# Performance work log

Measured on AMD Instinct MI355X. Metric: run time of the kernel, lower is better.

The kernel has to match this reference:

```python
import jax, jax.numpy as jnp
import numpy as np

E, H, B, S = 1024, 16, 8, 512
D = E // H
GRU_BIAS = 2.0  # config['gru_bias']
LN_EPS = 1e-5


def _pos_encoding(seq_len, dim):
    # Transformer-XL style relative positions seq_len-1 .. 0
    pos = jnp.arange(seq_len - 1, -1, -1, dtype=jnp.float32)
    inv_freq = 1.0 / (10000.0 ** (jnp.arange(0, dim, 2, dtype=jnp.float32) / dim))
    ang = pos[:, None] * inv_freq[None, :]              # [S, E/2]
    return jnp.concatenate([jnp.sin(ang), jnp.cos(ang)], axis=-1)  # [S, E]


def _layer_norm(x, g, b):
    m = x.mean(-1, keepdims=True)
    v = ((x - m) ** 2).mean(-1, keepdims=True)
    return (x - m) * jax.lax.rsqrt(v + LN_EPS) * g + b


def _rel_shift(x):
    # x: [B, H, S, S] -> Transformer-XL relative shift
    b, h, s, _ = x.shape
    x = jnp.pad(x, ((0, 0), (0, 0), (0, 0), (1, 0)))
    x = x.reshape(b, h, s + 1, s)[:, :, 1:, :]
    return x


def _gru_gate(x, y, Wr, Ur, Wz, Uz, Wg, Ug):
    # GTrXL gating: r, z gates + candidate h; z biased toward identity by GRU_BIAS
    r = jax.nn.sigmoid(y @ Wr.T + x @ Ur.T)
    z = jax.nn.sigmoid(y @ Wz.T + x @ Uz.T - GRU_BIAS)
    h = jnp.tanh(y @ Wg.T + (r * x) @ Ug.T)
    return (1.0 - z) * x + z * h


def setup_inputs() -> dict:
    rng = jax.random.key(0)
    ks = iter(jax.random.split(rng, 64))
    W = lambda *shape: jax.random.normal(next(ks), shape, jnp.float32) * 0.02
    inp = {
        "query": jax.random.normal(next(ks), (B, S, E), jnp.float32),
        "key": jax.random.normal(next(ks), (B, S, E), jnp.float32),
        "value": jax.random.normal(next(ks), (B, S, E), jnp.float32),
        "mask": jnp.tril(jnp.ones((S, S), dtype=bool)),
        "ln1_g": jnp.ones((E,), jnp.float32), "ln1_b": jnp.zeros((E,), jnp.float32),
        "ln2_g": jnp.ones((E,), jnp.float32), "ln2_b": jnp.zeros((E,), jnp.float32),
        "Wq": W(E, E), "bq": jnp.zeros((E,), jnp.float32),
        "Wk": W(E, E), "bk": jnp.zeros((E,), jnp.float32),
        "Wv": W(E, E), "bv": jnp.zeros((E,), jnp.float32),
        "Wp": W(E, E),
        "Wo": W(E, E), "bo": jnp.zeros((E,), jnp.float32),
        "u_bias": W(H, D), "v_bias": W(H, D),
        "g1_Wr": W(E, E), "g1_Ur": W(E, E), "g1_Wz": W(E, E),
        "g1_Uz": W(E, E), "g1_Wg": W(E, E), "g1_Ug": W(E, E),
        "g2_Wr": W(E, E), "g2_Ur": W(E, E), "g2_Wz": W(E, E),
        "g2_Uz": W(E, E), "g2_Wg": W(E, E), "g2_Ug": W(E, E),
        "fc_W": W(E, E), "fc_b": jnp.zeros((E,), jnp.float32),
    }
    return inp


def reference(query, key, value, mask,
              ln1_g, ln1_b, ln2_g, ln2_b,
              Wq, bq, Wk, bk, Wv, bv, Wp, Wo, bo, u_bias, v_bias,
              g1_Wr, g1_Ur, g1_Wz, g1_Uz, g1_Wg, g1_Ug,
              g2_Wr, g2_Ur, g2_Wz, g2_Uz, g2_Wg, g2_Ug,
              fc_W, fc_b):
    b, s, e = query.shape
    norm_q = _layer_norm(query, ln1_g, ln1_b)
    norm_k = _layer_norm(key, ln1_g, ln1_b)

    q = (norm_q @ Wq.T + bq).reshape(b, s, H, D)
    k = (norm_k @ Wk.T + bk).reshape(b, s, H, D)
    v = (norm_k @ Wv.T + bv).reshape(b, s, H, D)
    r = (_pos_encoding(s, e) @ Wp.T).reshape(s, H, D)      # relative pos keys

    # content term (q + u) k^T and position term (q + v) R^T with rel-shift
    AC = jnp.einsum('bshd,bthd->bhst', q + u_bias, k)
    BD = _rel_shift(jnp.einsum('bshd,thd->bhst', q + v_bias, r))
    score = (AC + BD) / jnp.sqrt(jnp.float32(D))
    score = jnp.where(mask[None, None, :, :], score, jnp.float32(-1e9))
    attn = jax.nn.softmax(score, axis=-1)
    Y = jnp.einsum('bhst,bthd->bshd', attn, v).reshape(b, s, e) @ Wo.T + bo

    out = _gru_gate(query, Y, g1_Wr, g1_Ur, g1_Wz, g1_Uz, g1_Wg, g1_Ug)
    Ef = jax.nn.relu(_layer_norm(out, ln2_g, ln2_b) @ fc_W.T + fc_b)
    out = _gru_gate(out, Ef, g2_Wr, g2_Ur, g2_Wz, g2_Uz, g2_Wg, g2_Ug)
    return out
```

## Files before the change

kernel.cpp:

```cpp
#include <hip/hip_runtime.h>

typedef unsigned short u16;
typedef __attribute__((ext_vector_type(8))) short short8;
typedef __attribute__((ext_vector_type(4))) float f32x4;

#define DEVFN __device__ __forceinline__

constexpr int Bc = 8, Sc = 512, Ec = 1024, Hc = 16, Dc = 64;

DEVFN u16 f2b(float f) {
  union { float f; unsigned u; } a; a.f = f;
  unsigned u = a.u;
  u += 0x7fffu + ((u >> 16) & 1u);
  return (u16)(u >> 16);
}
DEVFN float b2f(u16 h) {
  union { unsigned u; float f; } a; a.u = ((unsigned)h) << 16; return a.f;
}
DEVFN unsigned pack2(float a, float b) {
  return (unsigned)f2b(a) | ((unsigned)f2b(b) << 16);
}
DEVFN float wred_sum(float v) {
  #pragma unroll
  for (int o = 32; o; o >>= 1) v += __shfl_xor(v, o, 64);
  return v;
}
DEVFN void gload16(const void* g, void* l) {
  __builtin_amdgcn_global_load_lds(
      (const __attribute__((address_space(1))) void*)g,
      (__attribute__((address_space(3))) void*)l, 16, 0, 0);
}

struct PtrBundle { const float* src[18]; u16* dst[18]; };

__global__ __launch_bounds__(256) void cvtw_kernel(PtrBundle pb)
{
  int w = blockIdx.y;
  int i = blockIdx.x * 256 + threadIdx.x;
  float4 v = ((const float4*)pb.src[w])[i];
  uint2 o; o.x = pack2(v.x, v.y); o.y = pack2(v.z, v.w);
  ((uint2*)pb.dst[w])[i] = o;
}

struct GemmSeg {
  const u16* A1; const u16* A2;
  const u16* W1; const u16* W2;
  const float* bias;
  const float* bu; const float* bv;
  const u16* xB;
  const float* xF;
  const u16* zB;
  u16* o16a; u16* o16b;
  float* oF;
  int epi;
};
struct GemmDesc { GemmSeg seg[3]; };

template<int TM, int TN>
__global__ __launch_bounds__(TM == 128 ? 512 : 256) void gemm_f(GemmDesc dd)
{
  constexpr int MI = TM / 32;
  constexpr int D = (TM == 128) ? 2 : 3;
  constexpr int NBUF = D + 1;
  constexpr int BPS = 1024 / TN;
  __shared__ u16 lA[NBUF][TM * 32];
  __shared__ u16 lB[NBUF][TN * 32];
  const int tid = threadIdx.x;

  const GemmSeg s = dd.seg[blockIdx.y / BPS];
  const int n0 = (blockIdx.y % BPS) * TN;
  const int m0 = blockIdx.x * TM;
  const int wid = tid >> 6, lane = tid & 63;
  int wm, wn;
  if constexpr (TM == 128) { wm = (wid >> 2) * 64; wn = (wid & 3) * 32; }
  else                     { wm = (wid >> 1) * 32; wn = (wid & 1) * 32; }
  const int c15 = lane & 15, g = lane >> 4;
  const int arow = tid >> 2;
  const int ac8 = (((tid & 3) ^ ((tid >> 3) & 3))) * 8;
  const int gs8 = (g ^ ((c15 >> 1) & 3)) * 8;

  f32x4 acc[MI][2];
  #pragma unroll
  for (int mi = 0; mi < MI; ++mi)
    #pragma unroll
    for (int ni = 0; ni < 2; ++ni) acc[mi][ni] = {0.f, 0.f, 0.f, 0.f};

  const int nst = (s.A2 ? 2 : 1) * 32;

  auto stage = [&](int buf, int st) {
    int sg = st >> 5, k0 = (st & 31) << 5;
    const u16* Abase = (sg ? s.A2 : s.A1) + (size_t)m0 * 1024;
    const u16* Wbase = (sg ? s.W2 : s.W1) + (size_t)n0 * 1024;
    gload16(Abase + (size_t)arow * 1024 + k0 + ac8, &lA[buf][tid * 8]);
    gload16(Wbase + (size_t)arow * 1024 + k0 + ac8, &lB[buf][tid * 8]);
  };

  #pragma unroll
  for (int p = 0; p < D; ++p) stage(p, p);

  for (int st = 0; st < nst; ++st) {
    const int cur = st % NBUF;
    if constexpr (D == 2) {
      if (st + 1 < nst) asm volatile("s_waitcnt vmcnt(2)" ::: "memory");
      else              asm volatile("s_waitcnt vmcnt(0)" ::: "memory");
    } else {
      if (st + 2 < nst)      asm volatile("s_waitcnt vmcnt(4)" ::: "memory");
      else if (st + 1 < nst) asm volatile("s_waitcnt vmcnt(2)" ::: "memory");
      else                   asm volatile("s_waitcnt vmcnt(0)" ::: "memory");
    }
    __builtin_amdgcn_s_barrier();
    __builtin_amdgcn_sched_barrier(0);

    short8 afr[MI], bfr[2];
    #pragma unroll
    for (int mi = 0; mi < MI; ++mi)
      afr[mi] = *(const short8*)&lA[cur][(wm + mi * 16 + c15) * 32 + gs8];
    #pragma unroll
    for (int ni = 0; ni < 2; ++ni)
      bfr[ni] = *(const short8*)&lB[cur][(wn + ni * 16 + c15) * 32 + gs8];

    if (st + D < nst) stage((st + D) % NBUF, st + D);

    #pragma unroll
    for (int mi = 0; mi < MI; ++mi)
      #pragma unroll
      for (int ni = 0; ni < 2; ++ni)
        acc[mi][ni] = __builtin_amdgcn_mfma_f32_16x16x32_bf16(
            afr[mi], bfr[ni], acc[mi][ni], 0, 0, 0);
  }

  const int colb = n0 + wn + c15;
  const int rowb = m0 + wm + (lane >> 4) * 4;
  #pragma unroll
  for (int ni = 0; ni < 2; ++ni) {
    int col = colb + ni * 16;
    float bb = s.bias ? s.bias[col] : 0.f;
    float bu = 0.f, bvv = 0.f;
    if (s.epi == 1) { bu = s.bu[col]; bvv = s.bv[col]; }
    int hI = col >> 6, dI = col & 63;
    int kcd = (dI >> 5) & 1, gd = (dI >> 3) & 3, ed = dI & 7;
    int ntd = dI >> 4, c15d = dI & 15;
    #pragma unroll
    for (int mi = 0; mi < MI; ++mi) {
      int row0 = rowb + mi * 16;
      size_t off0 = (size_t)row0 * 1024 + col;
      float v4[4];
      #pragma unroll
      for (int q = 0; q < 4; ++q) v4[q] = acc[mi][ni][q] + bb;
      switch (s.epi) {
        case 0:
          #pragma unroll
          for (int q = 0; q < 4; ++q) s.o16a[off0 + (size_t)q * 1024] = f2b(v4[q]);
          break;
        case 1:
          #pragma unroll
          for (int q = 0; q < 4; ++q) {
            int ri = row0 + q;
            size_t off = ((size_t)hI << 18) +
                         (((size_t)(((ri >> 4) * 2 + kcd) * 16 + (ri & 15)) * 4 + gd) << 3) + ed;
            s.o16a[off] = f2b((v4[q] + bu)  * 0.125f);
            s.o16b[off] = f2b((v4[q] + bvv) * 0.125f);
          }
          break;
        case 2:
          #pragma unroll
          for (int q = 0; q < 4; ++q) s.o16a[off0 + (size_t)q * 1024] = f2b(v4[q]);
          break;
        case 3:
          #pragma unroll
          for (int q = 0; q < 4; ++q) {
            size_t off = off0 + (size_t)q * 1024;
            float sg1 = 1.f / (1.f + __expf(-v4[q]));
            s.o16a[off] = f2b(sg1 * b2f(s.xB[off]));
          }
          break;
        case 4:
          #pragma unroll
          for (int q = 0; q < 4; ++q) {
            size_t off = off0 + (size_t)q * 1024;
            float z = 1.f / (1.f + __expf(-(b2f(s.zB[off]) - 2.f)));
            float r = (1.f - z) * s.xF[off] + z * tanhf(v4[q]);
            s.oF[off] = r;
            if (s.o16a) s.o16a[off] = f2b(r);
          }
          break;
        case 5:
          #pragma unroll
          for (int q = 0; q < 4; ++q) s.o16a[off0 + (size_t)q * 1024] = f2b(fmaxf(v4[q], 0.f));
          break;
        case 6: {
          int bI = row0 >> 9, j = row0 & 511;
          int kt = j >> 6, jj = j & 63;
          int kcj = jj >> 5, gj = (jj >> 3) & 3, e0 = jj & 7;
          size_t off = ((size_t)((bI * 16 + hI) * 8 + kt) << 12) +
                       (((size_t)((ntd * 2 + kcj) * 16 + c15d) * 4 + gj) << 3) + e0;
          uint2 o; o.x = pack2(v4[0], v4[1]); o.y = pack2(v4[2], v4[3]);
          *(uint2*)(s.o16a + off) = o;
        } break;
        case 7:
          #pragma unroll
          for (int q = 0; q < 4; ++q) {
            int rj = row0 + q;
            int bI = rj >> 9, kt = (rj >> 6) & 7, jr = rj & 63;
            size_t off = ((size_t)((bI * 16 + hI) * 8 + kt) << 12) +
                         (((size_t)(((jr >> 4) * 2 + kcd) * 16 + (jr & 15)) * 4 + gd) << 3) + ed;
            s.o16a[off] = f2b(v4[q]);
          }
          break;
        case 8:
          #pragma unroll
          for (int q = 0; q < 4; ++q) {
            int t = row0 + q;
            size_t off = ((size_t)hI << 14) +
                         (((size_t)(((t >> 4) * 2 + kcd) * 16 + (t & 15)) * 4 + gd) << 3) + ed;
            s.o16a[off] = f2b(v4[q]);
          }
          break;
      }
    }
  }
}

__global__ __launch_bounds__(256) void ln_kernel(
    const float* __restrict__ x, const float* __restrict__ g,
    const float* __restrict__ bb, u16* __restrict__ out,
    u16* __restrict__ out2)
{
  const int row = blockIdx.x, t = threadIdx.x;
  float4 xv = ((const float4*)x)[(size_t)row * 256 + t];
  float s  = xv.x + xv.y + xv.z + xv.w;
  float s2 = xv.x * xv.x + xv.y * xv.y + xv.z * xv.z + xv.w * xv.w;
  s = wred_sum(s); s2 = wred_sum(s2);
  __shared__ float sh[8];
  int wid = t >> 6, lane = t & 63;
  if (lane == 0) { sh[wid] = s; sh[4 + wid] = s2; }
  __syncthreads();
  s  = sh[0] + sh[1] + sh[2] + sh[3];
  s2 = sh[4] + sh[5] + sh[6] + sh[7];
  float mean = s * (1.f / 1024.f);
  float var  = s2 * (1.f / 1024.f) - mean * mean;
  float rstd = rsqrtf(var + 1e-5f);
  float4 gv = ((const float4*)g)[t];
  float4 bv = ((const float4*)bb)[t];
  uint2 o;
  o.x = pack2((xv.x - mean) * rstd * gv.x + bv.x,
              (xv.y - mean) * rstd * gv.y + bv.y);
  o.y = pack2((xv.z - mean) * rstd * gv.z + bv.z,
              (xv.w - mean) * rstd * gv.w + bv.w);
  *(uint2*)&out[(size_t)row * 1024 + t * 4] = o;
  if (out2) {
    uint2 o2; o2.x = pack2(xv.x, xv.y); o2.y = pack2(xv.z, xv.w);
    *(uint2*)&out2[(size_t)row * 1024 + t * 4] = o2;
  }
}

__global__ __launch_bounds__(256) void posenc_kernel(u16* __restrict__ out)
{
  int idx = blockIdx.x * 256 + threadIdx.x;
  int i = idx >> 9, f = idx & 511;
  float pos = (float)(Sc - 1 - i);
  float invf = expf((float)f * -0.017988946039016f);
  float ang = pos * invf;
  out[(size_t)i * 1024 + f]       = f2b(sinf(ang));
  out[(size_t)i * 1024 + 512 + f] = f2b(cosf(ang));
}

__global__ __launch_bounds__(256) void attn_mfma(
    const u16* __restrict__ quF, const u16* __restrict__ qvF,
    const u16* __restrict__ PK, const u16* __restrict__ PVT,
    const u16* __restrict__ RF, u16* __restrict__ out)
{
  __shared__ u16 lK[2][4096];
  __shared__ u16 lVT[2][4096];
  __shared__ u16 PW[4][16 * 72];

  const int tid = threadIdx.x;
  const int wave = tid >> 6, lane = tid & 63;
  const int g = lane >> 4, c15 = lane & 15;
  const int x = blockIdx.x;
  const int h = blockIdx.y, b = blockIdx.z;
  const int qA = x, qB = 7 - x;

  const size_t pkbase = (size_t)(b * 16 + h) << 15;
  const size_t qhead  = (size_t)h << 18;
  const size_t rhead  = (size_t)h << 14;
  const size_t bh_off = ((size_t)b * Sc) * Ec + h * Dc;
  const int fchunk  = (c15 * 4 + g) * 8;
  const int fchunkS = (c15 * 4 + (g ^ ((c15 >> 1) & 3))) * 8;
  const int src8 = (tid ^ ((tid >> 3) & 3)) * 8;

  u16* pw = PW[wave];

  auto stage = [&](int buf, int kt) {
    const u16* ks = PK  + pkbase + ((size_t)kt << 12);
    const u16* vs = PVT + pkbase + ((size_t)kt << 12);
    gload16(ks + src8,        &lK[buf][tid * 8]);
    gload16(ks + 2048 + src8, &lK[buf][2048 + tid * 8]);
    gload16(vs + src8,        &lVT[buf][tid * 8]);
    gload16(vs + 2048 + src8, &lVT[buf][2048 + tid * 8]);
  };

  short8 qa[2], va[2];
  int i0w = qA * 64 + wave * 16;
  {
    int i16g = b * 32 + (i0w >> 4);
    #pragma unroll
    for (int kc = 0; kc < 2; ++kc) {
      size_t off = qhead + ((size_t)(i16g * 2 + kc) * 64) * 8 + fchunk;
      qa[kc] = *(const short8*)(quF + off);
      va[kc] = *(const short8*)(qvF + off);
    }
  }

  f32x4 oacc[4];
  #pragma unroll
  for (int t = 0; t < 4; ++t) oacc[t] = {0.f, 0.f, 0.f, 0.f};
  float m[4], l[4];
  #pragma unroll
  for (int q = 0; q < 4; ++q) { m[q] = -1e30f; l[q] = 0.f; }

  stage(0, 0);
  asm volatile("s_waitcnt vmcnt(0)" ::: "memory");
  __syncthreads();

  for (int s2 = 0; s2 < 9; ++s2) {
    const int buf = s2 & 1;
    const int kt = (s2 <= x) ? s2 : (s2 - x - 1);
    const int j0 = kt * 64;
    if (s2 < 8) {
      int ns = s2 + 1;
      stage(buf ^ 1, (ns <= x) ? ns : (ns - x - 1));
    }

    f32x4 ac[4];
    #pragma unroll
    for (int t = 0; t < 4; ++t) ac[t] = {0.f, 0.f, 0.f, 0.f};
    __builtin_amdgcn_s_setprio(1);
    #pragma unroll
    for (int kc = 0; kc < 2; ++kc)
      #pragma unroll
      for (int nt = 0; nt < 4; ++nt) {
        short8 kb = *(const short8*)&lK[buf][(nt * 2 + kc) * 512 + fchunkS];
        ac[nt] = __builtin_amdgcn_mfma_f32_16x16x32_bf16(qa[kc], kb, ac[nt], 0, 0, 0);
      }

    const int t016 = (496 - i0w + j0) >> 4;
    f32x4 e5[5];
    #pragma unroll
    for (int t = 0; t < 5; ++t) e5[t] = {0.f, 0.f, 0.f, 0.f};
    #pragma unroll
    for (int kc = 0; kc < 2; ++kc)
      #pragma unroll
      for (int nt = 0; nt < 5; ++nt) {
        int t16 = t016 + nt; t16 = t16 > 31 ? 31 : t16;
        short8 rb = *(const short8*)(RF + rhead + (size_t)(t16 * 2 + kc) * 512 + fchunk);
        e5[nt] = __builtin_amdgcn_mfma_f32_16x16x32_bf16(va[kc], rb, e5[nt], 0, 0, 0);
      }
    __builtin_amdgcn_s_setprio(0);

    float rot[5][4];
    #pragma unroll
    for (int q = 0; q < 4; ++q) {
      int src = (lane & 48) | ((15 - (g * 4 + q) + c15) & 15);
      #pragma unroll
      for (int nt = 0; nt < 5; ++nt)
        rot[nt][q] = __shfl(e5[nt][q], src, 64);
    }

    float s[4][4];
    #pragma unroll
    for (int ct = 0; ct < 4; ++ct) {
      int jcol = j0 + ct * 16 + c15;
      #pragma unroll
      for (int q = 0; q < 4; ++q) {
        int r = g * 4 + q;
        int u = 15 - r + c15;
        float bd = (u >> 4) ? rot[ct + 1][q] : rot[ct][q];
        float sv = ac[ct][q] + bd;
        s[ct][q] = (jcol <= i0w + r) ? sv : -1e30f;
      }
    }

    float mnew[4], csc[4];
    #pragma unroll
    for (int q = 0; q < 4; ++q) {
      float mx = fmaxf(fmaxf(s[0][q], s[1][q]), fmaxf(s[2][q], s[3][q]));
      #pragma unroll
      for (int o = 8; o; o >>= 1) mx = fmaxf(mx, __shfl_xor(mx, o, 64));
      mnew[q] = fmaxf(m[q], mx);
      csc[q] = __expf(m[q] - mnew[q]);
      m[q] = mnew[q];
    }
    float rs[4] = {0.f, 0.f, 0.f, 0.f};
    float p[4][4];
    #pragma unroll
    for (int ct = 0; ct < 4; ++ct)
      #pragma unroll
      for (int q = 0; q < 4; ++q) {
        p[ct][q] = __expf(s[ct][q] - mnew[q]);
        rs[q] += p[ct][q];
      }
    #pragma unroll
    for (int q = 0; q < 4; ++q) {
      float t = rs[q];
      #pragma unroll
      for (int o = 8; o; o >>= 1) t += __shfl_xor(t, o, 64);
      l[q] = l[q] * csc[q] + t;
      #pragma unroll
      for (int ct = 0; ct < 4; ++ct) oacc[ct][q] *= csc[q];
    }

    #pragma unroll
    for (int ct = 0; ct < 4; ++ct)
      #pragma unroll
      for (int q = 0; q < 4; ++q)
        pw[(g * 4 + q) * 72 + ct * 16 + c15] = f2b(p[ct][q]);

    __builtin_amdgcn_s_setprio(1);
    #pragma unroll
    for (int kc = 0; kc < 2; ++kc) {
      short8 pa = *(const short8*)&pw[c15 * 72 + kc * 32 + g * 8];
      #pragma unroll
      for (int nt = 0; nt < 4; ++nt) {
        short8 vb8 = *(const short8*)&lVT[buf][(nt * 2 + kc) * 512 + fchunkS];
        oacc[nt] = __builtin_amdgcn_mfma_f32_16x16x32_bf16(pa, vb8, oacc[nt], 0, 0, 0);
      }
    }
    __builtin_amdgcn_s_setprio(0);

    if (s2 == x) {
      #pragma unroll
      for (int q = 0; q < 4; ++q) {
        float rl = 1.f / l[q];
        size_t ro = bh_off + (size_t)(i0w + g * 4 + q) * Ec;
        #pragma unroll
        for (int ct = 0; ct < 4; ++ct)
          out[ro + ct * 16 + c15] = f2b(oacc[ct][q] * rl);
      }
      i0w = qB * 64 + wave * 16;
      int i16g = b * 32 + (i0w >> 4);
      #pragma unroll
      for (int kc = 0; kc < 2; ++kc) {
        size_t off = qhead + ((size_t)(i16g * 2 + kc) * 64) * 8 + fchunk;
        qa[kc] = *(const short8*)(quF + off);
        va[kc] = *(const short8*)(qvF + off);
      }
      #pragma unroll
      for (int t = 0; t < 4; ++t) oacc[t] = {0.f, 0.f, 0.f, 0.f};
      #pragma unroll
      for (int q = 0; q < 4; ++q) { m[q] = -1e30f; l[q] = 0.f; }
    }

    asm volatile("s_waitcnt vmcnt(0)" ::: "memory");
    __syncthreads();
  }

  #pragma unroll
  for (int q = 0; q < 4; ++q) {
    float rl = 1.f / l[q];
    size_t ro = bh_off + (size_t)(i0w + g * 4 + q) * Ec;
    #pragma unroll
    for (int ct = 0; ct < 4; ++ct)
      out[ro + ct * 16 + c15] = f2b(oacc[ct][q] * rl);
  }
}

extern "C" void kernel_launch(void* const* d_in, const int* in_sizes, int n_in,
                              void* d_out, int out_size, void* d_ws, size_t ws_size,
                              hipStream_t stream) {
  (void)in_sizes; (void)n_in; (void)out_size; (void)ws_size;

  const float* query = (const float*)d_in[0];
  const float* key   = (const float*)d_in[1];
  const float* ln1_g = (const float*)d_in[4];
  const float* ln1_b = (const float*)d_in[5];
  const float* ln2_g = (const float*)d_in[6];
  const float* ln2_b = (const float*)d_in[7];
  const float* Wq = (const float*)d_in[8];   const float* bq = (const float*)d_in[9];
  const float* Wk = (const float*)d_in[10];  const float* bk = (const float*)d_in[11];
  const float* Wv = (const float*)d_in[12];  const float* bv_in = (const float*)d_in[13];
  const float* Wp = (const float*)d_in[14];
  const float* Wo = (const float*)d_in[15];  const float* bo = (const float*)d_in[16];
  const float* u_bias = (const float*)d_in[17];
  const float* v_bias = (const float*)d_in[18];
  const float* fc_W = (const float*)d_in[31]; const float* fc_b = (const float*)d_in[32];

  const size_t MB = 1ull << 20;
  char* ws = (char*)d_ws;
  u16* wb[18];
  for (int i = 0; i < 18; ++i) wb[i] = (u16*)(ws + (size_t)i * 2 * MB);
  u16*   normq16 = (u16*)(ws + 36 * MB);
  u16*   normk16 = (u16*)(ws + 44 * MB);
  u16*   xq16    = (u16*)(ws + 52 * MB);
  u16*   pos16   = (u16*)(ws + 60 * MB);
  u16*   rF16    = (u16*)(ws + 61 * MB);
  u16*   quF16   = (u16*)(ws + 62 * MB);
  u16*   qvF16   = (u16*)(ws + 70 * MB);
  u16*   pk16    = (u16*)(ws + 78 * MB);
  u16*   pvt16   = (u16*)(ws + 86 * MB);
  float* out1    = (float*)(ws + 94 * MB);
  u16*   att16   = normq16;
  u16*   Y16     = normk16;
  u16*   rx16    = normq16;
  u16*   out116  = quF16;
  u16*   Ef16    = qvF16;
  u16*   ln2o16  = xq16;
  u16*   tB16    = pk16;

  PtrBundle pb;
  const float* wsrc[18] = {Wq, Wk, Wv, Wp, Wo, fc_W,
                           (const float*)d_in[19], (const float*)d_in[20],
                           (const float*)d_in[21], (const float*)d_in[22],
                           (const float*)d_in[23], (const float*)d_in[24],
                           (const float*)d_in[25], (const float*)d_in[26],
                           (const float*)d_in[27], (const float*)d_in[28],
                           (const float*)d_in[29], (const float*)d_in[30]};
  for (int i = 0; i < 18; ++i) { pb.src[i] = wsrc[i]; pb.dst[i] = wb[i]; }
  cvtw_kernel<<<dim3(1024, 18), 256, 0, stream>>>(pb);

  ln_kernel<<<4096, 256, 0, stream>>>(query, ln1_g, ln1_b, normq16, xq16);
  ln_kernel<<<4096, 256, 0, stream>>>(key,   ln1_g, ln1_b, normk16, nullptr);
  posenc_kernel<<<1024, 256, 0, stream>>>(pos16);

  GemmSeg z{}; GemmDesc d;

  d.seg[0] = z; d.seg[0].A1 = normq16; d.seg[0].W1 = wb[0]; d.seg[0].bias = bq;
  d.seg[0].bu = u_bias; d.seg[0].bv = v_bias;
  d.seg[0].o16a = quF16; d.seg[0].o16b = qvF16; d.seg[0].epi = 1;
  d.seg[1] = z; d.seg[1].A1 = normk16; d.seg[1].W1 = wb[1]; d.seg[1].bias = bk;
  d.seg[1].o16a = pk16; d.seg[1].epi = 7;
  d.seg[2] = z; d.seg[2].A1 = normk16; d.seg[2].W1 = wb[2]; d.seg[2].bias = bv_in;
  d.seg[2].o16a = pvt16; d.seg[2].epi = 6;
  gemm_f<128, 128><<<dim3(32, 24), 512, 0, stream>>>(d);

  d.seg[0] = z; d.seg[0].A1 = pos16; d.seg[0].W1 = wb[3];
  d.seg[0].o16a = rF16; d.seg[0].epi = 8;
  gemm_f<64, 64><<<dim3(8, 16), 256, 0, stream>>>(d);

  attn_mfma<<<dim3(4, 16, 8), 256, 0, stream>>>(quF16, qvF16, pk16, pvt16,
                                                rF16, att16);

  d.seg[0] = z; d.seg[0].A1 = att16; d.seg[0].W1 = wb[4]; d.seg[0].bias = bo;
  d.seg[0].o16a = Y16; d.seg[0].epi = 0;
  gemm_f<64, 64><<<dim3(64, 16), 256, 0, stream>>>(d);

  d.seg[0] = z; d.seg[0].A1 = Y16; d.seg[0].A2 = xq16;
  d.seg[0].W1 = wb[6]; d.seg[0].W2 = wb[7];
  d.seg[0].xB = xq16; d.seg[0].o16a = rx16; d.seg[0].epi = 3;
  d.seg[1] = z; d.seg[1].A1 = Y16; d.seg[1].A2 = xq16;
  d.seg[1].W1 = wb[8]; d.seg[1].W2 = wb[9];
  d.seg[1].o16a = tB16; d.seg[1].epi = 2;
  gemm_f<128, 128><<<dim3(32, 16), 512, 0, stream>>>(d);

  d.seg[0] = z; d.seg[0].A1 = Y16; d.seg[0].A2 = rx16;
  d.seg[0].W1 = wb[10]; d.seg[0].W2 = wb[11];
  d.seg[0].xF = query; d.seg[0].zB = tB16;
  d.seg[0].oF = out1; d.seg[0].o16a = out116; d.seg[0].epi = 4;
  gemm_f<64, 64><<<dim3(64, 16), 256, 0, stream>>>(d);

  ln_kernel<<<4096, 256, 0, stream>>>(out1, ln2_g, ln2_b, ln2o16, nullptr);
  d.seg[0] = z; d.seg[0].A1 = ln2o16; d.seg[0].W1 = wb[5]; d.seg[0].bias = fc_b;
  d.seg[0].o16a = Ef16; d.seg[0].epi = 5;
  gemm_f<64, 64><<<dim3(64, 16), 256, 0, stream>>>(d);

  d.seg[0] = z; d.seg[0].A1 = Ef16; d.seg[0].A2 = out116;
  d.seg[0].W1 = wb[12]; d.seg[0].W2 = wb[13];
  d.seg[0].xB = out116; d.seg[0].o16a = rx16; d.seg[0].epi = 3;
  d.seg[1] = z; d.seg[1].A1 = Ef16; d.seg[1].A2 = out116;
  d.seg[1].W1 = wb[14]; d.seg[1].W2 = wb[15];
  d.seg[1].o16a = tB16; d.seg[1].epi = 2;
  gemm_f<128, 128><<<dim3(32, 16), 512, 0, stream>>>(d);

  d.seg[0] = z; d.seg[0].A1 = Ef16; d.seg[0].A2 = rx16;
  d.seg[0].W1 = wb[16]; d.seg[0].W2 = wb[17];
  d.seg[0].xF = out1; d.seg[0].zB = tB16;
  d.seg[0].oF = (float*)d_out; d.seg[0].epi = 4;
  gemm_f<64, 64><<<dim3(64, 16), 256, 0, stream>>>(d);
}
```

Baseline: 329.2 us.

## Load GEMM A operand directly from global into registers, bypassing LDS

The GEMM kernel no longer stages the activation (A) tile through shared memory. Each wave now loads its A fragments straight from global memory into registers, one k-step ahead, while weights stay in a 3-buffer LDS ring with prefetch distance 2 and the wait counts are adjusted to match. The goal is to cut LDS footprint and LDS write/read traffic for A. The cost is that waves sharing the same rows each fetch A separately, which raises global/L2 traffic. The loads are also narrow 64-byte-per-row accesses with only one stage of latency hiding.

```diff
diff --git a/kernel.cpp b/kernel.cpp
--- a/kernel.cpp
+++ b/kernel.cpp
@@ -60,11 +60,8 @@
 __global__ __launch_bounds__(TM == 128 ? 512 : 256) void gemm_f(GemmDesc dd)
 {
   constexpr int MI = TM / 32;
-  constexpr int D = (TM == 128) ? 2 : 3;
-  constexpr int NBUF = D + 1;
   constexpr int BPS = 1024 / TN;
-  __shared__ u16 lA[NBUF][TM * 32];
-  __shared__ u16 lB[NBUF][TN * 32];
+  __shared__ u16 lB[3][TN * 32];
   const int tid = threadIdx.x;
 
   const GemmSeg s = dd.seg[blockIdx.y / BPS];
@@ -75,10 +72,14 @@
   if constexpr (TM == 128) { wm = (wid >> 2) * 64; wn = (wid & 3) * 32; }
   else                     { wm = (wid >> 1) * 32; wn = (wid & 1) * 32; }
   const int c15 = lane & 15, g = lane >> 4;
-  const int arow = tid >> 2;
   const int ac8 = (((tid & 3) ^ ((tid >> 3) & 3))) * 8;
   const int gs8 = (g ^ ((c15 >> 1) & 3)) * 8;
 
+  size_t aoff[MI];
+  #pragma unroll
+  for (int mi = 0; mi < MI; ++mi)
+    aoff[mi] = (size_t)(m0 + wm + mi * 16 + c15) * 1024 + g * 8;
+
   f32x4 acc[MI][2];
   #pragma unroll
   for (int mi = 0; mi < MI; ++mi)
@@ -87,46 +88,49 @@
 
   const int nst = (s.A2 ? 2 : 1) * 32;
 
-  auto stage = [&](int buf, int st) {
+  auto wstage = [&](int buf, int st) {
     int sg = st >> 5, k0 = (st & 31) << 5;
-    const u16* Abase = (sg ? s.A2 : s.A1) + (size_t)m0 * 1024;
     const u16* Wbase = (sg ? s.W2 : s.W1) + (size_t)n0 * 1024;
-    gload16(Abase + (size_t)arow * 1024 + k0 + ac8, &lA[buf][tid * 8]);
-    gload16(Wbase + (size_t)arow * 1024 + k0 + ac8, &lB[buf][tid * 8]);
+    gload16(Wbase + (size_t)(tid >> 2) * 1024 + k0 + ac8, &lB[buf][tid * 8]);
   };
-
-  #pragma unroll
-  for (int p = 0; p < D; ++p) stage(p, p);
-
+  auto aload = [&](int st, short8* dst) {
+    int sg = st >> 5, k0 = (st & 31) << 5;
+    const u16* Abase = sg ? s.A2 : s.A1;
+    #pragma unroll
+    for (int mi = 0; mi < MI; ++mi)
+      dst[mi] = *(const short8*)(Abase + aoff[mi] + k0);
+  };
+
+  short8 cura[MI], nexta[MI];
+  aload(0, cura);
+  wstage(0, 0);
+  wstage(1, 1);
+
+  #pragma unroll 2
   for (int st = 0; st < nst; ++st) {
-    const int cur = st % NBUF;
-    if constexpr (D == 2) {
-      if (st + 1 < nst) asm volatile("s_waitcnt vmcnt(2)" ::: "memory");
-      else              asm volatile("s_waitcnt vmcnt(0)" ::: "memory");
-    } else {
-      if (st + 2 < nst)      asm volatile("s_waitcnt vmcnt(4)" ::: "memory");
-      else if (st + 1 < nst) asm volatile("s_waitcnt vmcnt(2)" ::: "memory");
-      else                   asm volatile("s_waitcnt vmcnt(0)" ::: "memory");
-    }
+    const int cur = st % 3;
+    if (st + 1 < nst) asm volatile("s_waitcnt vmcnt(1)" ::: "memory");
+    else              asm volatile("s_waitcnt vmcnt(0)" ::: "memory");
     __builtin_amdgcn_s_barrier();
     __builtin_amdgcn_sched_barrier(0);
 
-    short8 afr[MI], bfr[2];
-    #pragma unroll
-    for (int mi = 0; mi < MI; ++mi)
-      afr[mi] = *(const short8*)&lA[cur][(wm + mi * 16 + c15) * 32 + gs8];
+    short8 bfr[2];
     #pragma unroll
     for (int ni = 0; ni < 2; ++ni)
       bfr[ni] = *(const short8*)&lB[cur][(wn + ni * 16 + c15) * 32 + gs8];
 
-    if (st + D < nst) stage((st + D) % NBUF, st + D);
+    if (st + 1 < nst) aload(st + 1, nexta);
+    if (st + 2 < nst) wstage((st + 2) % 3, st + 2);
 
     #pragma unroll
     for (int mi = 0; mi < MI; ++mi)
       #pragma unroll
       for (int ni = 0; ni < 2; ++ni)
         acc[mi][ni] = __builtin_amdgcn_mfma_f32_16x16x32_bf16(
-            afr[mi], bfr[ni], acc[mi][ni], 0, 0, 0);
+            cura[mi], bfr[ni], acc[mi][ni], 0, 0, 0);
+
+    #pragma unroll
+    for (int mi = 0; mi < MI; ++mi) cura[mi] = nexta[mi];
   }
 
   const int colb = n0 + wn + c15;
```

Measured after the change: 678.1 us. 2.06x slower.
